# Optimization experiments

Hardware: AMD Instinct MI355X
Metric: run time of the kernel (lower is better)

## Reference

```python
import jax, jax.numpy as jnp
import numpy as np

DIM = 2560
HEADS = 64
HEAD_DIM = 40
TEMB = 512
FF = 4 * DIM
B = 1
S = 1248
TXT = 224
EPS = 1e-6


def _ln(x, eps=EPS):
    # LayerNorm over last dim, no affine (elementwise_affine=False)
    m = jnp.mean(x, axis=-1, keepdims=True)
    v = jnp.mean(jnp.square(x - m), axis=-1, keepdims=True)
    return (x - m) * jax.lax.rsqrt(v + eps)


def setup_inputs() -> dict:
    key = jax.random.key(0)
    ks = jax.random.split(key, 10)
    w = 0.02
    return {
        "hidden_states": jax.random.normal(ks[0], (B, S, DIM), jnp.float32),
        "emb": jax.random.normal(ks[1], (B, TEMB), jnp.float32),
        "attention_mask": jnp.zeros((B, 1, S, S), jnp.float32),
        "adaln_w": jax.random.normal(ks[2], (TEMB, 12 * DIM), jnp.float32) * w,
        "adaln_b": jnp.zeros((12 * DIM,), jnp.float32),
        "qkv_w": jax.random.normal(ks[3], (DIM, 3 * DIM), jnp.float32) * w,
        "qkv_b": jnp.zeros((3 * DIM,), jnp.float32),
        "out_w": jax.random.normal(ks[4], (DIM, DIM), jnp.float32) * w,
        "out_b": jnp.zeros((DIM,), jnp.float32),
        "ff1_w": jax.random.normal(ks[5], (DIM, FF), jnp.float32) * w,
        "ff1_b": jnp.zeros((FF,), jnp.float32),
        "ff2_w": jax.random.normal(ks[6], (FF, DIM), jnp.float32) * w,
        "ff2_b": jnp.zeros((DIM,), jnp.float32),
        "text_length": TXT,
    }


def reference(hidden_states, emb, attention_mask, adaln_w, adaln_b, qkv_w, qkv_b,
              out_w, out_b, ff1_w, ff1_b, ff2_w, ff2_b, text_length):
    b, s, d = hidden_states.shape
    t = text_length

    # adaLN: SiLU -> Linear(time_embed_dim, 12*dim), chunk into 12 [B, dim] pieces
    ada = jax.nn.silu(emb) @ adaln_w + adaln_b
    (sh_msa_i, sc_msa_i, g_msa_i, sh_mlp_i, sc_mlp_i, g_mlp_i,
     sh_msa_t, sc_msa_t, g_msa_t, sh_mlp_t, sc_mlp_t, g_mlp_t) = jnp.split(ada, 12, axis=1)

    def mod(x, shift, scale):
        return x * (1.0 + scale[:, None, :]) + shift[:, None, :]

    # --- attention block ---
    ai = _ln(hidden_states)
    ai = jnp.concatenate([mod(ai[:, :t], sh_msa_t, sc_msa_t),
                          mod(ai[:, t:], sh_msa_i, sc_msa_i)], axis=1)

    qkv = ai @ qkv_w + qkv_b                              # [B, S, 3*D]
    q, k, v = jnp.split(qkv, 3, axis=-1)
    q = q.reshape(b, s, HEADS, HEAD_DIM).transpose(0, 2, 1, 3)  # [B, H, S, hd]
    k = k.reshape(b, s, HEADS, HEAD_DIM).transpose(0, 2, 1, 3)
    v = v.reshape(b, s, HEADS, HEAD_DIM).transpose(0, 2, 1, 3)

    q = _ln(q)  # per-head QK layernorm
    k = _ln(k)

    scores = jnp.einsum("bhqd,bhkd->bhqk", q, k) / (HEAD_DIM ** 0.5)
    scores = scores + attention_mask
    probs = jax.nn.softmax(scores, axis=-1)
    ctx = jnp.einsum("bhqk,bhkd->bhqd", probs, v)
    ctx = ctx.transpose(0, 2, 1, 3).reshape(b, s, d)
    attn_out = ctx @ out_w + out_b

    h = jnp.concatenate([hidden_states[:, :t] + g_msa_t[:, None, :] * attn_out[:, :t],
                         hidden_states[:, t:] + g_msa_i[:, None, :] * attn_out[:, t:]], axis=1)

    # --- MLP block ---
    mi = _ln(h)
    mi = jnp.concatenate([mod(mi[:, :t], sh_mlp_t, sc_mlp_t),
                          mod(mi[:, t:], sh_mlp_i, sc_mlp_i)], axis=1)
    mo = jax.nn.gelu(mi @ ff1_w + ff1_b, approximate=True) @ ff2_w + ff2_b

    h = jnp.concatenate([h[:, :t] + g_mlp_t[:, None, :] * mo[:, :t],
                         h[:, t:] + g_mlp_i[:, None, :] * mo[:, t:]], axis=1)
    return h
```

## Files before the change

### kernel.cpp

```cpp
#include <hip/hip_runtime.h>
#include <cstdint>

typedef float f32x4 __attribute__((ext_vector_type(4)));
typedef __bf16 bf16x8 __attribute__((ext_vector_type(8)));
typedef __bf16 bf16x4 __attribute__((ext_vector_type(4)));

#define S_LEN 1248
#define S_PAD 1280
#define DIMD 2560
#define NHEAD 64
#define HDIM 40
#define T3 7680

__device__ __forceinline__ f32x4 mfma16(bf16x8 a, bf16x8 b, f32x4 c) {
  return __builtin_amdgcn_mfma_f32_16x16x32_bf16(a, b, c, 0, 0, 0);
}


__device__ __forceinline__ void dev_trans(int vbid, const float* __restrict__ W,
                                          __bf16* __restrict__ Wt, int K, int N, char* smraw) {
  float (*t)[65] = (float(*)[65])smraw;
  int gxt = N >> 6;
  int n0 = (vbid % gxt) * 64, k0 = (vbid / gxt) * 64;
  int tid = threadIdx.x;
  #pragma unroll
  for (int i = 0; i < 4; ++i) {
    int r = i * 16 + (tid >> 4), c = (tid & 15) * 4;
    const float4 v = *(const float4*)&W[(size_t)(k0 + r) * N + n0 + c];
    t[r][c] = v.x; t[r][c + 1] = v.y; t[r][c + 2] = v.z; t[r][c + 3] = v.w;
  }
  __syncthreads();
  #pragma unroll
  for (int j = 0; j < 4; ++j) {
    int n = j * 16 + (tid >> 4), kk = (tid & 15) * 4;
    bf16x4 o;
    o[0] = (__bf16)t[kk][n];     o[1] = (__bf16)t[kk + 1][n];
    o[2] = (__bf16)t[kk + 2][n]; o[3] = (__bf16)t[kk + 3][n];
    *(bf16x4*)&Wt[(size_t)(n0 + n) * K + k0 + kk] = o;
  }
}

__device__ __forceinline__ void dev_lnmod(int row, const float* __restrict__ X,
                                          const float* __restrict__ ada,
                                          int csh_t, int csc_t, int csh_i, int csc_i,
                                          const int* __restrict__ tlp,
                                          __bf16* __restrict__ Y, char* smraw) {
  float* rs = (float*)smraw;
  float* rq = rs + 4;
  int tid = threadIdx.x;
  const float* x = X + (size_t)row * DIMD;
  float v[10], s = 0.f, s2 = 0.f;
  #pragma unroll
  for (int i = 0; i < 10; ++i) { v[i] = x[tid + i * 256]; s += v[i]; s2 += v[i] * v[i]; }
  #pragma unroll
  for (int m = 1; m < 64; m <<= 1) { s += __shfl_xor(s, m, 64); s2 += __shfl_xor(s2, m, 64); }
  if ((tid & 63) == 0) { rs[tid >> 6] = s; rq[tid >> 6] = s2; }
  __syncthreads();
  s = rs[0] + rs[1] + rs[2] + rs[3];
  s2 = rq[0] + rq[1] + rq[2] + rq[3];
  float mean = s * (1.f / DIMD);
  float rstd = rsqrtf(s2 * (1.f / DIMD) - mean * mean + 1e-6f);
  int txt = *tlp;
  int csh = row < txt ? csh_t : csh_i, csc = row < txt ? csc_t : csc_i;
  #pragma unroll
  for (int i = 0; i < 10; ++i) {
    int col = tid + i * 256;
    float y = (v[i] - mean) * rstd;
    y = y * (1.f + ada[csc * DIMD + col]) + ada[csh * DIMD + col];
    Y[(size_t)row * DIMD + col] = (__bf16)y;
  }
}

template <int EPI>
__device__ __forceinline__ void dev_gemm(int vbid, unsigned gx, unsigned gy, unsigned gz,
                                         const __bf16* __restrict__ A, int lda,
                                         const __bf16* __restrict__ Bt, int ldb,
                                         const float* __restrict__ bias, int N, int ksize,
                                         float* __restrict__ Cf, float* __restrict__ Cp,
                                         __bf16* __restrict__ Cb, char* smraw) {
  __bf16 (*smem)[2][4096] = (__bf16(*)[2][4096])smraw;
  int tid = threadIdx.x;

  unsigned nwg = gx * gy * gz;
  unsigned orig = (unsigned)vbid;
  unsigned qq = nwg >> 3, r8 = nwg & 7;
  unsigned xcd = orig & 7, loc = orig >> 3;
  unsigned swz = (xcd < r8 ? xcd * (qq + 1) : r8 * (qq + 1) + (xcd - r8) * qq) + loc;
  unsigned bx = swz % gx;
  unsigned rest = swz / gx;
  unsigned by = rest % gy;
  unsigned bz = rest / gy;

  int m0 = bx * 128, n0 = by * 128;
  int kbase = bz * ksize;
  int wave = tid >> 6, lane = tid & 63;
  int wm = (wave & 1) * 64, wn = (wave >> 1) * 64;
  int l15 = lane & 15, l4 = lane >> 4;
  f32x4 acc[4][4] = {};

  auto STG = [&](__bf16* As, __bf16* Bs, int kk) {
    #pragma unroll
    for (int i = 0; i < 2; ++i) {
      int c = tid + i * 256;
      int row = c >> 2, ko = (c & 3) * 8;
      __builtin_amdgcn_global_load_lds(
          (const __attribute__((address_space(1))) unsigned int*)(A + (size_t)(m0 + row) * lda + kk + ko),
          (__attribute__((address_space(3))) unsigned int*)(As + c * 8), 16, 0, 0);
      __builtin_amdgcn_global_load_lds(
          (const __attribute__((address_space(1))) unsigned int*)(Bt + (size_t)(n0 + row) * ldb + kk + ko),
          (__attribute__((address_space(3))) unsigned int*)(Bs + c * 8), 16, 0, 0);
    }
  };

  int nt = ksize >> 5;
  STG(smem[0][0], smem[0][1], kbase);
  STG(smem[1][0], smem[1][1], kbase + 32);
  asm volatile("s_waitcnt vmcnt(4)" ::: "memory");
  __builtin_amdgcn_s_barrier();

  int rb = 0, sb = 2;
  for (int t = 0; t < nt; ++t) {
    if (t + 2 < nt) STG(smem[sb][0], smem[sb][1], kbase + (t + 2) * 32);
    const __bf16* As = smem[rb][0];
    const __bf16* Bs = smem[rb][1];
    bf16x8 af[4], bfr[4];
    #pragma unroll
    for (int s = 0; s < 4; ++s) {
      af[s] = *(const bf16x8*)&As[(wm + s * 16 + l15) * 32 + l4 * 8];
      bfr[s] = *(const bf16x8*)&Bs[(wn + s * 16 + l15) * 32 + l4 * 8];
    }
    __builtin_amdgcn_s_setprio(1);
    #pragma unroll
    for (int i = 0; i < 4; ++i)
      #pragma unroll
      for (int j = 0; j < 4; ++j)
        acc[i][j] = mfma16(af[i], bfr[j], acc[i][j]);
    __builtin_amdgcn_s_setprio(0);
    __builtin_amdgcn_sched_barrier(0);
    if (t + 2 < nt)
      asm volatile("s_waitcnt vmcnt(4)" ::: "memory");
    else
      asm volatile("s_waitcnt vmcnt(0)" ::: "memory");
    __builtin_amdgcn_s_barrier();
    rb = rb == 2 ? 0 : rb + 1;
    sb = sb == 2 ? 0 : sb + 1;
  }

  float* Cfo = Cf;
  if constexpr (EPI == 3) Cfo = (bz == 0) ? Cf : (Cp + (size_t)(bz - 1) * S_PAD * N);
  #pragma unroll
  for (int i = 0; i < 4; ++i) {
    #pragma unroll
    for (int r = 0; r < 4; ++r) {
      int rr = m0 + wm + i * 16 + l4 * 4 + r;
      if (rr >= S_LEN) continue;
      #pragma unroll
      for (int j = 0; j < 4; ++j) {
        int col = n0 + wn + j * 16 + l15;
        if constexpr (EPI == 0) {
          Cfo[(size_t)rr * N + col] = acc[i][j][r] + bias[col];
        } else if constexpr (EPI == 3) {
          Cfo[(size_t)rr * N + col] = acc[i][j][r];
        } else if constexpr (EPI == 4) {
          Cb[(size_t)rr * N + col] = (__bf16)(acc[i][j][r] + bias[col]);
        } else {
          float val = acc[i][j][r] + bias[col];
          float u = val + 0.044715f * val * val * val;
          float gl = 0.5f * val * (1.f + tanhf(0.7978845608028654f * u));
          Cb[(size_t)rr * N + col] = (__bf16)gl;
        }
      }
    }
  }
}

__device__ void dev_attn(int vbid, const __bf16* __restrict__ Qb,
                         const __bf16* __restrict__ Kb, const __bf16* __restrict__ Vt,
                         const float* __restrict__ mask, __bf16* __restrict__ ctx,
                         char* smraw) {
  __bf16 (*kvs)[2][4096] = (__bf16(*)[2][4096])smraw;
  __bf16 (*plds)[2][1024] = (__bf16(*)[2][1024])(smraw + 32768);
  unsigned orig = (unsigned)vbid;
  unsigned swz = (orig & 7) * 80 + (orig >> 3);
  int h = swz / 10, q0 = (swz % 10) * 128;
  int tid = threadIdx.x, wave = tid >> 6, lane = tid & 63;
  int l15 = lane & 15, l4 = lane >> 4;
  int qb = q0 + wave * 32;

  const __bf16* Kh = Kb + (size_t)h * S_PAD * 64;
  const __bf16* Vh = Vt + (size_t)h * 64 * S_PAD;

  auto STAGE = [&](int buf, int kv0) {
    #pragma unroll
    for (int i = 0; i < 2; ++i) {
      int c = tid + i * 256;
      int row = c >> 3, col = ((c & 7) ^ (row & 7)) * 8;
      __builtin_amdgcn_global_load_lds(
          (const __attribute__((address_space(1))) unsigned int*)(Kh + (size_t)(kv0 + row) * 64 + col),
          (__attribute__((address_space(3))) unsigned int*)&kvs[buf][0][c * 8], 16, 0, 0);
      __builtin_amdgcn_global_load_lds(
          (const __attribute__((address_space(1))) unsigned int*)(Vh + (size_t)row * S_PAD + kv0 + col),
          (__attribute__((address_space(3))) unsigned int*)&kvs[buf][1][c * 8], 16, 0, 0);
    }
  };

  bf16x8 qf[2][2];
  #pragma unroll
  for (int g = 0; g < 2; ++g) {
    const __bf16* Qp = Qb + ((size_t)h * S_PAD + qb + g * 16 + l15) * 64 + l4 * 8;
    qf[g][0] = *(const bf16x8*)Qp;
    qf[g][1] = *(const bf16x8*)(Qp + 32);
  }
  const float* mrow[2][4];
  #pragma unroll
  for (int g = 0; g < 2; ++g)
    #pragma unroll
    for (int r = 0; r < 4; ++r) {
      int qr = qb + g * 16 + l4 * 4 + r;
      mrow[g][r] = mask + (size_t)(qr < S_LEN ? qr : S_LEN - 1) * S_LEN;
    }
  f32x4 o[2][3] = {};

  STAGE(0, 0);
  for (int t = 0; t < 20; ++t) {
    int kv0 = t * 64;
    if (t < 19) {
      STAGE((t + 1) & 1, kv0 + 64);
      asm volatile("s_waitcnt vmcnt(4)" ::: "memory");
    } else {
      asm volatile("s_waitcnt vmcnt(0)" ::: "memory");
    }
    __builtin_amdgcn_s_barrier();
    const __bf16* Ks = kvs[t & 1][0];
    const __bf16* Vs = kvs[t & 1][1];

    float mreg[2][4][4];
    #pragma unroll
    for (int g = 0; g < 2; ++g)
      #pragma unroll
      for (int ns = 0; ns < 4; ++ns) {
        int kvc = kv0 + ns * 16 + l15;
        int mc = kvc < S_LEN ? kvc : S_LEN - 1;
        #pragma unroll
        for (int r = 0; r < 4; ++r) mreg[g][ns][r] = mrow[g][r][mc];
      }

    bf16x8 kf[4][2];
    #pragma unroll
    for (int ns = 0; ns < 4; ++ns) {
      int kvr = ns * 16 + l15, sw = kvr & 7;
      kf[ns][0] = *(const bf16x8*)((const char*)Ks + kvr * 128 + ((l4 ^ sw) << 4));
      kf[ns][1] = *(const bf16x8*)((const char*)Ks + kvr * 128 + (((4 + l4) ^ sw) << 4));
    }
    bf16x8 vf[3][2];
    #pragma unroll
    for (int d3 = 0; d3 < 3; ++d3) {
      int dr = d3 * 16 + l15, sw = dr & 7;
      vf[d3][0] = *(const bf16x8*)((const char*)Vs + dr * 128 + ((l4 ^ sw) << 4));
      vf[d3][1] = *(const bf16x8*)((const char*)Vs + dr * 128 + (((4 + l4) ^ sw) << 4));
    }

    #pragma unroll
    for (int g = 0; g < 2; ++g) {
      f32x4 sf[4];
      #pragma unroll
      for (int ns = 0; ns < 4; ++ns) {
        f32x4 a = {};
        a = mfma16(qf[g][0], kf[ns][0], a);
        a = mfma16(qf[g][1], kf[ns][1], a);
        sf[ns] = a;
      }
      #pragma unroll
      for (int ns = 0; ns < 4; ++ns) {
        int kvc = kv0 + ns * 16 + l15;
        #pragma unroll
        for (int r = 0; r < 4; ++r) {
          float val = sf[ns][r] - 8.f + mreg[g][ns][r];
          if (kvc >= S_LEN) val = -100.f;
          float e = __expf(val);
          int prow = l4 * 4 + r;
          int boff = (prow * 128 + (ns * 16 + l15) * 2) ^ ((prow & 7) << 4);
          plds[wave][g][boff >> 1] = (__bf16)e;
        }
      }
      int swp = (l15 & 7) << 4;
      int ba = l15 * 128 + l4 * 16;
      bf16x8 pa0 = *(const bf16x8*)((const char*)plds[wave][g] + (ba ^ swp));
      bf16x8 pa1 = *(const bf16x8*)((const char*)plds[wave][g] + ((ba + 64) ^ swp));
      #pragma unroll
      for (int d3 = 0; d3 < 3; ++d3) {
        o[g][d3] = mfma16(pa0, vf[d3][0], o[g][d3]);
        o[g][d3] = mfma16(pa1, vf[d3][1], o[g][d3]);
      }
    }
    __builtin_amdgcn_s_barrier();
  }

  #pragma unroll
  for (int g = 0; g < 2; ++g) {
    #pragma unroll
    for (int r = 0; r < 4; ++r) {
      float sum = __shfl(o[g][2][r], (lane & 0x30) + 8, 64);
      float rinv = 1.f / sum;
      int qr = qb + g * 16 + l4 * 4 + r;
      if (qr < S_LEN) {
        #pragma unroll
        for (int d3 = 0; d3 < 3; ++d3) {
          int d = d3 * 16 + l15;
          if (d < HDIM)
            ctx[(size_t)qr * DIMD + h * HDIM + d] = (__bf16)(o[g][d3][r] * rinv);
        }
      }
    }
  }
}


__global__ void k_adaln(const float* __restrict__ emb, const float* __restrict__ W,
                        const float* __restrict__ b, float* __restrict__ ada) {
  __shared__ __attribute__((aligned(16))) float se[512];
  int tid = threadIdx.x;
  for (int i = tid; i < 512; i += 64) {
    float e = emb[i];
    se[i] = e / (1.f + __expf(-e));
  }
  __syncthreads();
  int col = blockIdx.x * 64 + tid;
  float acc = 0.f;
  #pragma unroll 8
  for (int k = 0; k < 512; ++k) acc += se[k] * W[(size_t)k * 30720 + col];
  ada[col] = acc + b[col];
}

__global__ __launch_bounds__(256) void k_lnmod_qtrans(const float* __restrict__ X,
                                                      const float* __restrict__ ada,
                                                      const int* __restrict__ tlp,
                                                      __bf16* __restrict__ Y,
                                                      const float* __restrict__ W,
                                                      __bf16* __restrict__ Wt) {
  __shared__ __attribute__((aligned(16))) char sm[16640];
  int b = blockIdx.x;
  if (b < 1248) dev_lnmod(b, X, ada, 6, 7, 0, 1, tlp, Y, sm);
  else dev_trans(b - 1248, W, Wt, 2560, 7680, sm);
}

__global__ __launch_bounds__(256) void k_lnmod(const float* __restrict__ X,
                                               const float* __restrict__ ada,
                                               int csh_t, int csc_t, int csh_i, int csc_i,
                                               const int* __restrict__ tlp,
                                               __bf16* __restrict__ Y) {
  __shared__ __attribute__((aligned(16))) char sm[64];
  dev_lnmod(blockIdx.x, X, ada, csh_t, csc_t, csh_i, csc_i, tlp, Y, sm);
}

template <int EPI>
__global__ __launch_bounds__(256) void k_gemm_trans(
    const __bf16* __restrict__ A, int lda, const __bf16* __restrict__ Bt, int ldb,
    const float* __restrict__ bias, int N, int ksize,
    float* __restrict__ Cf, float* __restrict__ Cp, __bf16* __restrict__ Cb,
    unsigned gx, unsigned gy, unsigned gz,
    const float* __restrict__ W, __bf16* __restrict__ Wt, int tK, int tN) {
  __shared__ __attribute__((aligned(16))) char sm[49152];
  int b = blockIdx.x;
  int split = (int)(gx * gy * gz);
  if (b < split) dev_gemm<EPI>(b, gx, gy, gz, A, lda, Bt, ldb, bias, N, ksize, Cf, Cp, Cb, sm);
  else dev_trans(b - split, W, Wt, tK, tN, sm);
}

template <int EPI>
__global__ __launch_bounds__(256) void k_gemm(
    const __bf16* __restrict__ A, int lda, const __bf16* __restrict__ Bt, int ldb,
    const float* __restrict__ bias, int N, int ksize,
    float* __restrict__ Cf, float* __restrict__ Cp, __bf16* __restrict__ Cb) {
  __shared__ __attribute__((aligned(16))) char sm[49152];
  int vbid = (blockIdx.z * gridDim.y + blockIdx.y) * gridDim.x + blockIdx.x;
  dev_gemm<EPI>(vbid, gridDim.x, gridDim.y, gridDim.z, A, lda, Bt, ldb, bias, N, ksize,
                Cf, Cp, Cb, sm);
}

__global__ __launch_bounds__(256) void k_attn_trans(const __bf16* __restrict__ Qb,
                                                    const __bf16* __restrict__ Kb,
                                                    const __bf16* __restrict__ Vt,
                                                    const float* __restrict__ mask,
                                                    __bf16* __restrict__ ctx,
                                                    const float* __restrict__ W,
                                                    __bf16* __restrict__ Wt, int tK, int tN) {
  __shared__ __attribute__((aligned(16))) char sm[49152];
  int b = blockIdx.x;
  if (b < 640) dev_attn(b, Qb, Kb, Vt, mask, ctx, sm);
  else dev_trans(b - 640, W, Wt, tK, tN, sm);
}

template <int NS>
__global__ __launch_bounds__(256) void k_red(const float* __restrict__ p0,
                                             const float* __restrict__ prest,
                                             const float* __restrict__ bias,
                                             const float* __restrict__ resid,
                                             const float* __restrict__ ada,
                                             int g_t, int g_i, const int* __restrict__ tlp,
                                             int N, float* __restrict__ out) {
  int idx = blockIdx.x * 256 + threadIdx.x;
  int perRow = N >> 2;
  int row = idx / perRow;
  int c4 = (idx - row * perRow) << 2;
  if (row >= S_LEN) return;
  int txt = *tlp;
  size_t off = (size_t)row * N + c4;
  float4 s = *(const float4*)&p0[off];
  #pragma unroll
  for (int z = 0; z < NS - 1; ++z) {
    const float4 p = *(const float4*)&prest[(size_t)z * S_PAD * N + off];
    s.x += p.x; s.y += p.y; s.z += p.z; s.w += p.w;
  }
  const float4 bb = *(const float4*)&bias[c4];
  const float4 rr = *(const float4*)&resid[off];
  const float4 gg = *(const float4*)&ada[(size_t)(row < txt ? g_t : g_i) * DIMD + c4];
  float4 o;
  o.x = rr.x + gg.x * (s.x + bb.x);
  o.y = rr.y + gg.y * (s.y + bb.y);
  o.z = rr.z + gg.z * (s.z + bb.z);
  o.w = rr.w + gg.w * (s.w + bb.w);
  *(float4*)&out[off] = o;
}

__global__ __launch_bounds__(128) void k_qkln(const __bf16* __restrict__ qkv,
                                              __bf16* __restrict__ Qb, __bf16* __restrict__ Kb) {
  __shared__ __attribute__((aligned(16))) float buf[5120];
  int srow = blockIdx.x, tid = threadIdx.x;
  const __bf16* rowp = qkv + (size_t)srow * T3;
  for (int i = tid; i < 640; i += 128) {
    bf16x8 v = *(const bf16x8*)&rowp[i * 8];
    #pragma unroll
    for (int j = 0; j < 8; ++j) buf[i * 8 + j] = (float)v[j];
  }
  __syncthreads();
  int h = tid & 63;
  bool isK = tid >= 64;
  const float* x = buf + (isK ? DIMD : 0) + h * HDIM;
  float xv[40], s = 0.f;
  #pragma unroll
  for (int d = 0; d < 40; ++d) { xv[d] = x[d]; s += xv[d]; }
  float mean = s * (1.f / 40.f);
  float s2 = 0.f;
  #pragma unroll
  for (int d = 0; d < 40; ++d) { float t = xv[d] - mean; s2 += t * t; }
  float rstd = rsqrtf(s2 * (1.f / 40.f) + 1e-6f);
  float scale = isK ? rstd : rstd * 0.15811388300841897f;
  __bf16* dst = (isK ? Kb : Qb) + ((size_t)h * S_PAD + srow) * 64;
  #pragma unroll
  for (int i = 0; i < 5; ++i) {
    bf16x8 w;
    #pragma unroll
    for (int j = 0; j < 8; ++j) w[j] = (__bf16)((xv[i * 8 + j] - mean) * scale);
    *(bf16x8*)&dst[i * 8] = w;
  }
  bf16x8 z = {};
  *(bf16x8*)&dst[40] = z;
  *(bf16x8*)&dst[48] = z;
  *(bf16x8*)&dst[56] = z;
}

__global__ __launch_bounds__(256) void k_vtrans(const __bf16* __restrict__ qkv,
                                                __bf16* __restrict__ Vt) {
  __shared__ __attribute__((aligned(16))) float t[64][41];
  int h = blockIdx.y, s0 = blockIdx.x * 64;
  int tid = threadIdx.x;
  for (int i = tid; i < 64 * 40; i += 256) {
    int sr = i / 40, d = i - sr * 40;
    int srow = s0 + sr;
    t[sr][d] = (srow < S_LEN) ? (float)qkv[(size_t)srow * T3 + 2 * DIMD + h * HDIM + d] : 0.f;
  }
  __syncthreads();
  int d = tid >> 2, sc = (tid & 3) * 16;
  bf16x8 w0 = {}, w1 = {};
  if (d < 40) {
    #pragma unroll
    for (int q = 0; q < 8; ++q) {
      w0[q] = (__bf16)t[sc + q][d];
      w1[q] = (__bf16)t[sc + 8 + q][d];
    }
  } else if (d == 40) {
    #pragma unroll
    for (int q = 0; q < 8; ++q) { w0[q] = (__bf16)1.0f; w1[q] = (__bf16)1.0f; }
  }
  __bf16* dst = Vt + ((size_t)h * 64 + d) * S_PAD + s0 + sc;
  *(bf16x8*)&dst[0] = w0;
  *(bf16x8*)&dst[8] = w1;
}

extern "C" void kernel_launch(void* const* d_in, const int* in_sizes, int n_in,
                              void* d_out, int out_size, void* d_ws, size_t ws_size,
                              hipStream_t stream) {
  const float* hidden  = (const float*)d_in[0];
  const float* emb     = (const float*)d_in[1];
  const float* mask    = (const float*)d_in[2];
  const float* adaln_w = (const float*)d_in[3];
  const float* adaln_b = (const float*)d_in[4];
  const float* qkv_w   = (const float*)d_in[5];
  const float* qkv_b   = (const float*)d_in[6];
  const float* out_w   = (const float*)d_in[7];
  const float* out_b   = (const float*)d_in[8];
  const float* ff1_w   = (const float*)d_in[9];
  const float* ff1_b   = (const float*)d_in[10];
  const float* ff2_w   = (const float*)d_in[11];
  const float* ff2_b   = (const float*)d_in[12];
  const int*   tl      = (const int*)d_in[13];
  (void)in_sizes; (void)n_in; (void)out_size; (void)ws_size;

  char* w = (char*)d_ws;
  size_t off = 0;
  auto alloc = [&](size_t b) { char* p = w + off; off += (b + 255) & ~(size_t)255; return p; };
  float*  ada  = (float*)alloc(30720 * 4);
  __bf16* wTf1 = (__bf16*)alloc((size_t)10240 * 2560 * 2);
  __bf16* wTq2 = (__bf16*)alloc((size_t)10240 * 2560 * 2);
  __bf16* ai   = (__bf16*)alloc((size_t)S_PAD * DIMD * 2);
  __bf16* actB = (__bf16*)alloc((size_t)S_PAD * 10240 * 2);
  __bf16* Qb   = (__bf16*)alloc((size_t)NHEAD * S_PAD * 64 * 2);
  __bf16* Kb   = (__bf16*)alloc((size_t)NHEAD * S_PAD * 64 * 2);
  __bf16* Vt   = (__bf16*)alloc((size_t)NHEAD * 64 * S_PAD * 2);
  __bf16* ctxb = (__bf16*)alloc((size_t)S_PAD * DIMD * 2);
  float*  hbuf = (float*)alloc((size_t)S_PAD * DIMD * 4);
  __bf16* mi    = ai;
  __bf16* qkvB  = actB;
  __bf16* ff1o  = actB;
  __bf16* wTo   = (__bf16*)hbuf;
  float*  partO = (float*)Qb;
  float*  partF = (float*)Qb;

  k_adaln<<<dim3(480), dim3(64), 0, stream>>>(emb, adaln_w, adaln_b, ada);
  k_lnmod_qtrans<<<dim3(1248 + 4800), dim3(256), 0, stream>>>(hidden, ada, tl, ai, qkv_w, wTq2);
  k_gemm_trans<4><<<dim3(600 + 1600), dim3(256), 0, stream>>>(
      ai, 2560, wTq2, 2560, qkv_b, 7680, 2560, nullptr, nullptr, qkvB,
      10, 60, 1, out_w, wTo, 2560, 2560);
  k_qkln<<<dim3(1248), dim3(128), 0, stream>>>(qkvB, Qb, Kb);
  k_vtrans<<<dim3(20, 64), dim3(256), 0, stream>>>(qkvB, Vt);
  k_attn_trans<<<dim3(640 + 6400), dim3(256), 0, stream>>>(Qb, Kb, Vt, mask, ctxb,
                                                           ff1_w, wTf1, 2560, 10240);
  k_gemm_trans<3><<<dim3(400 + 6400), dim3(256), 0, stream>>>(
      ctxb, 2560, wTo, 2560, nullptr, 2560, 1280, partO, partO + (size_t)S_PAD * 2560, nullptr,
      10, 20, 2, ff2_w, wTq2, 10240, 2560);
  k_red<2><<<dim3(3120), dim3(256), 0, stream>>>(partO, partO + (size_t)S_PAD * 2560, out_b,
                                                 hidden, ada, 8, 2, tl, 2560, hbuf);
  k_lnmod<<<dim3(1248), dim3(256), 0, stream>>>(hbuf, ada, 9, 10, 3, 4, tl, mi);
  k_gemm<2><<<dim3(10, 80, 1), dim3(256), 0, stream>>>(mi, 2560, wTf1, 2560, ff1_b, 10240, 2560,
                                                       nullptr, nullptr, ff1o);
  k_gemm<3><<<dim3(10, 20, 2), dim3(256), 0, stream>>>(ff1o, 10240, wTq2, 10240, nullptr, 2560, 5120,
                                                       partF, partF + (size_t)S_PAD * 2560, nullptr);
  k_red<2><<<dim3(3120), dim3(256), 0, stream>>>(partF, partF + (size_t)S_PAD * 2560, ff2_b,
                                                 hbuf, ada, 11, 5, tl, 2560, (float*)d_out);
}
```

Baseline: 540.9 us.

## Fuse QK-LN with V transpose, split-K reduce with LayerNorm, and move ff2 transpose

Merges the per-head QK layernorm and V transpose into one launch. Fuses the out-proj split-K reduction, residual gating and the MLP LayerNorm/modulation into a single per-row kernel, which drops a separate LN pass over hbuf. Moves the ff2 weight transpose from the out-proj GEMM launch to the ff1 GEMM launch, so the small out-proj GEMM runs alone and the transpose overlaps a larger GEMM. The fused LN computes variance as E[x^2]-mean^2 in one pass, which is slightly less numerically robust.

```diff
diff --git a/kernel.cpp b/kernel.cpp
--- a/kernel.cpp
+++ b/kernel.cpp
@@ -344,15 +344,6 @@
   else dev_trans(b - 1248, W, Wt, 2560, 7680, sm);
 }
 
-__global__ __launch_bounds__(256) void k_lnmod(const float* __restrict__ X,
-                                               const float* __restrict__ ada,
-                                               int csh_t, int csc_t, int csh_i, int csc_i,
-                                               const int* __restrict__ tlp,
-                                               __bf16* __restrict__ Y) {
-  __shared__ __attribute__((aligned(16))) char sm[64];
-  dev_lnmod(blockIdx.x, X, ada, csh_t, csc_t, csh_i, csc_i, tlp, Y, sm);
-}
-
 template <int EPI>
 __global__ __launch_bounds__(256) void k_gemm_trans(
     const __bf16* __restrict__ A, int lda, const __bf16* __restrict__ Bt, int ldb,
@@ -391,101 +382,143 @@
   else dev_trans(b - 640, W, Wt, tK, tN, sm);
 }
 
-template <int NS>
-__global__ __launch_bounds__(256) void k_red(const float* __restrict__ p0,
-                                             const float* __restrict__ prest,
-                                             const float* __restrict__ bias,
-                                             const float* __restrict__ resid,
-                                             const float* __restrict__ ada,
-                                             int g_t, int g_i, const int* __restrict__ tlp,
-                                             int N, float* __restrict__ out) {
+__global__ __launch_bounds__(256) void k_qkvprep(const __bf16* __restrict__ qkv,
+                                                 __bf16* __restrict__ Qb,
+                                                 __bf16* __restrict__ Kb,
+                                                 __bf16* __restrict__ Vt) {
+  __shared__ __attribute__((aligned(16))) char sm[40960];
+  int b = blockIdx.x, tid = threadIdx.x;
+  if (b < 624) {
+    float (*buf)[5120] = (float(*)[5120])sm;
+    int sub = tid >> 7, t2 = tid & 127;
+    int srow = b * 2 + sub;
+    const __bf16* rowp = qkv + (size_t)srow * T3;
+    for (int i = t2; i < 640; i += 128) {
+      bf16x8 v = *(const bf16x8*)&rowp[i * 8];
+      #pragma unroll
+      for (int j = 0; j < 8; ++j) buf[sub][i * 8 + j] = (float)v[j];
+    }
+    __syncthreads();
+    int h = t2 & 63;
+    bool isK = t2 >= 64;
+    const float* x = buf[sub] + (isK ? DIMD : 0) + h * HDIM;
+    float xv[40], s = 0.f;
+    #pragma unroll
+    for (int d = 0; d < 40; ++d) { xv[d] = x[d]; s += xv[d]; }
+    float mean = s * (1.f / 40.f);
+    float s2 = 0.f;
+    #pragma unroll
+    for (int d = 0; d < 40; ++d) { float t = xv[d] - mean; s2 += t * t; }
+    float rstd = rsqrtf(s2 * (1.f / 40.f) + 1e-6f);
+    float scale = isK ? rstd : rstd * 0.15811388300841897f;
+    __bf16* dst = (isK ? Kb : Qb) + ((size_t)h * S_PAD + srow) * 64;
+    #pragma unroll
+    for (int i = 0; i < 5; ++i) {
+      bf16x8 w;
+      #pragma unroll
+      for (int j = 0; j < 8; ++j) w[j] = (__bf16)((xv[i * 8 + j] - mean) * scale);
+      *(bf16x8*)&dst[i * 8] = w;
+    }
+    bf16x8 z = {};
+    *(bf16x8*)&dst[40] = z;
+    *(bf16x8*)&dst[48] = z;
+    *(bf16x8*)&dst[56] = z;
+  } else {
+    float (*t)[41] = (float(*)[41])sm;
+    int vbid = b - 624;
+    int h = vbid / 20, s0 = (vbid % 20) * 64;
+    for (int i = tid; i < 64 * 40; i += 256) {
+      int sr = i / 40, d = i - sr * 40;
+      int srow = s0 + sr;
+      t[sr][d] = (srow < S_LEN) ? (float)qkv[(size_t)srow * T3 + 2 * DIMD + h * HDIM + d] : 0.f;
+    }
+    __syncthreads();
+    int d = tid >> 2, sc = (tid & 3) * 16;
+    bf16x8 w0 = {}, w1 = {};
+    if (d < 40) {
+      #pragma unroll
+      for (int q = 0; q < 8; ++q) {
+        w0[q] = (__bf16)t[sc + q][d];
+        w1[q] = (__bf16)t[sc + 8 + q][d];
+      }
+    } else if (d == 40) {
+      #pragma unroll
+      for (int q = 0; q < 8; ++q) { w0[q] = (__bf16)1.0f; w1[q] = (__bf16)1.0f; }
+    }
+    __bf16* dst = Vt + ((size_t)h * 64 + d) * S_PAD + s0 + sc;
+    *(bf16x8*)&dst[0] = w0;
+    *(bf16x8*)&dst[8] = w1;
+  }
+}
+
+__global__ __launch_bounds__(256) void k_redln(const float* __restrict__ p0,
+                                               const float* __restrict__ p1,
+                                               const float* __restrict__ bias,
+                                               const float* __restrict__ resid,
+                                               const float* __restrict__ ada,
+                                               int g_t, int g_i,
+                                               int csh_t, int csc_t, int csh_i, int csc_i,
+                                               const int* __restrict__ tlp,
+                                               float* __restrict__ hout,
+                                               __bf16* __restrict__ Y) {
+  __shared__ float rs[4], rq[4];
+  int row = blockIdx.x, tid = threadIdx.x;
+  int txt = *tlp;
+  bool isTxt = row < txt;
+  size_t off = (size_t)row * DIMD;
+  const float* gp = ada + (size_t)(isTxt ? g_t : g_i) * DIMD;
+  float v[10], s = 0.f, s2 = 0.f;
+  #pragma unroll
+  for (int i = 0; i < 10; ++i) {
+    int col = tid + i * 256;
+    float val = p0[off + col] + p1[off + col] + bias[col];
+    float hh = resid[off + col] + gp[col] * val;
+    hout[off + col] = hh;
+    v[i] = hh; s += hh; s2 += hh * hh;
+  }
+  #pragma unroll
+  for (int m = 1; m < 64; m <<= 1) { s += __shfl_xor(s, m, 64); s2 += __shfl_xor(s2, m, 64); }
+  if ((tid & 63) == 0) { rs[tid >> 6] = s; rq[tid >> 6] = s2; }
+  __syncthreads();
+  s = rs[0] + rs[1] + rs[2] + rs[3];
+  s2 = rq[0] + rq[1] + rq[2] + rq[3];
+  float mean = s * (1.f / DIMD);
+  float rstd = rsqrtf(s2 * (1.f / DIMD) - mean * mean + 1e-6f);
+  int csh = isTxt ? csh_t : csh_i, csc = isTxt ? csc_t : csc_i;
+  #pragma unroll
+  for (int i = 0; i < 10; ++i) {
+    int col = tid + i * 256;
+    float y = (v[i] - mean) * rstd;
+    y = y * (1.f + ada[csc * DIMD + col]) + ada[csh * DIMD + col];
+    Y[off + col] = (__bf16)y;
+  }
+}
+
+__global__ __launch_bounds__(256) void k_red2(const float* __restrict__ p0,
+                                              const float* __restrict__ p1,
+                                              const float* __restrict__ bias,
+                                              const float* __restrict__ resid,
+                                              const float* __restrict__ ada,
+                                              int g_t, int g_i, const int* __restrict__ tlp,
+                                              float* __restrict__ out) {
   int idx = blockIdx.x * 256 + threadIdx.x;
-  int perRow = N >> 2;
+  int perRow = DIMD >> 2;
   int row = idx / perRow;
   int c4 = (idx - row * perRow) << 2;
   if (row >= S_LEN) return;
   int txt = *tlp;
-  size_t off = (size_t)row * N + c4;
-  float4 s = *(const float4*)&p0[off];
-  #pragma unroll
-  for (int z = 0; z < NS - 1; ++z) {
-    const float4 p = *(const float4*)&prest[(size_t)z * S_PAD * N + off];
-    s.x += p.x; s.y += p.y; s.z += p.z; s.w += p.w;
-  }
+  size_t off = (size_t)row * DIMD + c4;
+  const float4 a = *(const float4*)&p0[off];
+  const float4 p = *(const float4*)&p1[off];
   const float4 bb = *(const float4*)&bias[c4];
   const float4 rr = *(const float4*)&resid[off];
   const float4 gg = *(const float4*)&ada[(size_t)(row < txt ? g_t : g_i) * DIMD + c4];
   float4 o;
-  o.x = rr.x + gg.x * (s.x + bb.x);
-  o.y = rr.y + gg.y * (s.y + bb.y);
-  o.z = rr.z + gg.z * (s.z + bb.z);
-  o.w = rr.w + gg.w * (s.w + bb.w);
+  o.x = rr.x + gg.x * (a.x + p.x + bb.x);
+  o.y = rr.y + gg.y * (a.y + p.y + bb.y);
+  o.z = rr.z + gg.z * (a.z + p.z + bb.z);
+  o.w = rr.w + gg.w * (a.w + p.w + bb.w);
   *(float4*)&out[off] = o;
-}
-
-__global__ __launch_bounds__(128) void k_qkln(const __bf16* __restrict__ qkv,
-                                              __bf16* __restrict__ Qb, __bf16* __restrict__ Kb) {
-  __shared__ __attribute__((aligned(16))) float buf[5120];
-  int srow = blockIdx.x, tid = threadIdx.x;
-  const __bf16* rowp = qkv + (size_t)srow * T3;
-  for (int i = tid; i < 640; i += 128) {
-    bf16x8 v = *(const bf16x8*)&rowp[i * 8];
-    #pragma unroll
-    for (int j = 0; j < 8; ++j) buf[i * 8 + j] = (float)v[j];
-  }
-  __syncthreads();
-  int h = tid & 63;
-  bool isK = tid >= 64;
-  const float* x = buf + (isK ? DIMD : 0) + h * HDIM;
-  float xv[40], s = 0.f;
-  #pragma unroll
-  for (int d = 0; d < 40; ++d) { xv[d] = x[d]; s += xv[d]; }
-  float mean = s * (1.f / 40.f);
-  float s2 = 0.f;
-  #pragma unroll
-  for (int d = 0; d < 40; ++d) { float t = xv[d] - mean; s2 += t * t; }
-  float rstd = rsqrtf(s2 * (1.f / 40.f) + 1e-6f);
-  float scale = isK ? rstd : rstd * 0.15811388300841897f;
-  __bf16* dst = (isK ? Kb : Qb) + ((size_t)h * S_PAD + srow) * 64;
-  #pragma unroll
-  for (int i = 0; i < 5; ++i) {
-    bf16x8 w;
-    #pragma unroll
-    for (int j = 0; j < 8; ++j) w[j] = (__bf16)((xv[i * 8 + j] - mean) * scale);
-    *(bf16x8*)&dst[i * 8] = w;
-  }
-  bf16x8 z = {};
-  *(bf16x8*)&dst[40] = z;
-  *(bf16x8*)&dst[48] = z;
-  *(bf16x8*)&dst[56] = z;
-}
-
-__global__ __launch_bounds__(256) void k_vtrans(const __bf16* __restrict__ qkv,
-                                                __bf16* __restrict__ Vt) {
-  __shared__ __attribute__((aligned(16))) float t[64][41];
-  int h = blockIdx.y, s0 = blockIdx.x * 64;
-  int tid = threadIdx.x;
-  for (int i = tid; i < 64 * 40; i += 256) {
-    int sr = i / 40, d = i - sr * 40;
-    int srow = s0 + sr;
-    t[sr][d] = (srow < S_LEN) ? (float)qkv[(size_t)srow * T3 + 2 * DIMD + h * HDIM + d] : 0.f;
-  }
-  __syncthreads();
-  int d = tid >> 2, sc = (tid & 3) * 16;
-  bf16x8 w0 = {}, w1 = {};
-  if (d < 40) {
-    #pragma unroll
-    for (int q = 0; q < 8; ++q) {
-      w0[q] = (__bf16)t[sc + q][d];
-      w1[q] = (__bf16)t[sc + 8 + q][d];
-    }
-  } else if (d == 40) {
-    #pragma unroll
-    for (int q = 0; q < 8; ++q) { w0[q] = (__bf16)1.0f; w1[q] = (__bf16)1.0f; }
-  }
-  __bf16* dst = Vt + ((size_t)h * 64 + d) * S_PAD + s0 + sc;
-  *(bf16x8*)&dst[0] = w0;
-  *(bf16x8*)&dst[8] = w1;
 }
 
 extern "C" void kernel_launch(void* const* d_in, const int* in_sizes, int n_in,
@@ -532,20 +565,18 @@
   k_gemm_trans<4><<<dim3(600 + 1600), dim3(256), 0, stream>>>(
       ai, 2560, wTq2, 2560, qkv_b, 7680, 2560, nullptr, nullptr, qkvB,
       10, 60, 1, out_w, wTo, 2560, 2560);
-  k_qkln<<<dim3(1248), dim3(128), 0, stream>>>(qkvB, Qb, Kb);
-  k_vtrans<<<dim3(20, 64), dim3(256), 0, stream>>>(qkvB, Vt);
+  k_qkvprep<<<dim3(624 + 1280), dim3(256), 0, stream>>>(qkvB, Qb, Kb, Vt);
   k_attn_trans<<<dim3(640 + 6400), dim3(256), 0, stream>>>(Qb, Kb, Vt, mask, ctxb,
                                                            ff1_w, wTf1, 2560, 10240);
-  k_gemm_trans<3><<<dim3(400 + 6400), dim3(256), 0, stream>>>(
-      ctxb, 2560, wTo, 2560, nullptr, 2560, 1280, partO, partO + (size_t)S_PAD * 2560, nullptr,
-      10, 20, 2, ff2_w, wTq2, 10240, 2560);
-  k_red<2><<<dim3(3120), dim3(256), 0, stream>>>(partO, partO + (size_t)S_PAD * 2560, out_b,
-                                                 hidden, ada, 8, 2, tl, 2560, hbuf);
-  k_lnmod<<<dim3(1248), dim3(256), 0, stream>>>(hbuf, ada, 9, 10, 3, 4, tl, mi);
-  k_gemm<2><<<dim3(10, 80, 1), dim3(256), 0, stream>>>(mi, 2560, wTf1, 2560, ff1_b, 10240, 2560,
-                                                       nullptr, nullptr, ff1o);
+  k_gemm<3><<<dim3(10, 20, 2), dim3(256), 0, stream>>>(ctxb, 2560, wTo, 2560, nullptr, 2560, 1280,
+                                                       partO, partO + (size_t)S_PAD * 2560, nullptr);
+  k_redln<<<dim3(1248), dim3(256), 0, stream>>>(partO, partO + (size_t)S_PAD * 2560, out_b,
+                                                hidden, ada, 8, 2, 9, 10, 3, 4, tl, hbuf, mi);
+  k_gemm_trans<2><<<dim3(800 + 6400), dim3(256), 0, stream>>>(
+      mi, 2560, wTf1, 2560, ff1_b, 10240, 2560, nullptr, nullptr, ff1o,
+      10, 80, 1, ff2_w, wTq2, 10240, 2560);
   k_gemm<3><<<dim3(10, 20, 2), dim3(256), 0, stream>>>(ff1o, 10240, wTq2, 10240, nullptr, 2560, 5120,
                                                        partF, partF + (size_t)S_PAD * 2560, nullptr);
-  k_red<2><<<dim3(3120), dim3(256), 0, stream>>>(partF, partF + (size_t)S_PAD * 2560, ff2_b,
-                                                 hbuf, ada, 11, 5, tl, 2560, (float*)d_out);
-}
+  k_red2<<<dim3(3120), dim3(256), 0, stream>>>(partF, partF + (size_t)S_PAD * 2560, ff2_b,
+                                               hbuf, ada, 11, 5, tl, (float*)d_out);
+}
```

Result: faster. 513.5 us (median of 3 runs) (-5.1%).
